# Performance work log

Hardware: AMD Instinct MI355X
Metric: run time of the kernel (lower is better)

The kernel has to match this reference:

```python
import jax, jax.numpy as jnp
import numpy as np

WINDOW_SIZE = 11
C1 = 0.01 ** 2
C2 = 0.03 ** 2


def _box_filter(x, ws):
    # x: [B,1,H,W]; uniform box filter, zero padding (== torch conv2d pad=ws//2)
    k = jnp.full((1, 1, ws, ws), 1.0 / (ws * ws), dtype=x.dtype)
    pad = ws // 2
    return jax.lax.conv_general_dilated(
        x, k, window_strides=(1, 1), padding=[(pad, pad), (pad, pad)],
        dimension_numbers=('NCHW', 'OIHW', 'NCHW'))


def setup_inputs() -> dict:
    key = jax.random.key(0)
    k1, k2 = jax.random.split(key)
    img1 = jax.random.uniform(k1, (64, 1, 512, 512), dtype=jnp.float32)
    img2 = jax.random.uniform(k2, (64, 1, 512, 512), dtype=jnp.float32)
    return {"img1": img1, "img2": img2}


def reference(img1, img2):
    ws = WINDOW_SIZE
    mu1 = _box_filter(img1, ws)
    mu2 = _box_filter(img2, ws)
    mu1_sq = mu1 * mu1
    mu2_sq = mu2 * mu2
    mu1_mu2 = mu1 * mu2
    sigma1_sq = _box_filter(img1 * img1, ws) - mu1_sq
    sigma2_sq = _box_filter(img2 * img2, ws) - mu2_sq
    sigma12 = _box_filter(img1 * img2, ws) - mu1_mu2
    ssim_map = ((2 * mu1_mu2 + C1) * (2 * sigma12 + C2)) / (
        (mu1_sq + mu2_sq + C1) * (sigma1_sq + sigma2_sq + C2))
    return 1.0 - jnp.mean(ssim_map)
```

## Files before the change

kernel.cpp:

```cpp
#include <hip/hip_runtime.h>


#define IMG_H 512
#define IMG_W 512
#define N_IMG 64
#define STRIP 16
#define CHUNK 2
#define NTHREADS 128
#define SSZ 528
#define QSZ 132
#define ROWSZ (SSZ + QSZ)

__global__ __launch_bounds__(NTHREADS) void ssim_kernel(const float* __restrict__ img1,
                                                        const float* __restrict__ img2,
                                                        float* __restrict__ ws) {
    __shared__ __align__(16) float V[CHUNK][4][ROWSZ];
    __shared__ float wsum[2];
    const int t = threadIdx.x;
    const int b = blockIdx.y;
    const int r0 = blockIdx.x * STRIP;
    const float* __restrict__ p1 = img1 + (size_t)b * (IMG_H * IMG_W);
    const float* __restrict__ p2 = img2 + (size_t)b * (IMG_H * IMG_W);

    for (int i = t; i < CHUNK * 4 * ROWSZ; i += NTHREADS) (&V[0][0][0])[i] = 0.0f;

    const int c4 = 4 * t;
    float cs[4][4];
#pragma unroll
    for (int ch = 0; ch < 4; ++ch)
#pragma unroll
        for (int j = 0; j < 4; ++j) cs[ch][j] = 0.0f;

    auto addrow = [&](int r) {
        float4 x = *(const float4*)(p1 + (size_t)r * IMG_W + c4);
        float4 y = *(const float4*)(p2 + (size_t)r * IMG_W + c4);
        float xs[4] = {x.x, x.y, x.z, x.w}, ys[4] = {y.x, y.y, y.z, y.w};
#pragma unroll
        for (int j = 0; j < 4; ++j) {
            float u = xs[j] + ys[j], v = xs[j] - ys[j];
            cs[0][j] += u;                  cs[1][j] += v;
            cs[2][j] = fmaf(u, u, cs[2][j]); cs[3][j] = fmaf(v, v, cs[3][j]);
        }
    };
    auto subrow = [&](int r) {
        float4 x = *(const float4*)(p1 + (size_t)r * IMG_W + c4);
        float4 y = *(const float4*)(p2 + (size_t)r * IMG_W + c4);
        float xs[4] = {x.x, x.y, x.z, x.w}, ys[4] = {y.x, y.y, y.z, y.w};
#pragma unroll
        for (int j = 0; j < 4; ++j) {
            float u = xs[j] + ys[j], v = xs[j] - ys[j];
            cs[0][j] -= u;                  cs[1][j] -= v;
            cs[2][j] = fmaf(-u, u, cs[2][j]); cs[3][j] = fmaf(-v, v, cs[3][j]);
        }
    };

    int offS[4][3], offQ[4][2];
#pragma unroll
    for (int k = 0; k < 4; ++k) {
        const int c = t + 128 * k;
        const int rho = c & 3;
        int e0, e1, e2;
        if (rho == 0)      { e0 = -5; e1 =  4; e2 =  5; }
        else if (rho == 1) { e0 =  3; e1 =  4; e2 =  5; }
        else if (rho == 2) { e0 = -5; e1 = -4; e2 = -3; }
        else               { e0 = -5; e1 = -4; e2 =  5; }
        offS[k][0] = c + 8 + e0; offS[k][1] = c + 8 + e1; offS[k][2] = c + 8 + e2;
        const int mlo = (c >> 2) + ((rho < 2) ? -1 : 0);
        offQ[k][0] = SSZ + 2 + mlo; offQ[k][1] = SSZ + 3 + mlo;
    }

    {
        int rlo = r0 - 5; if (rlo < 0) rlo = 0;
        int rhi = r0 + 5; if (rhi > IMG_H - 1) rhi = IMG_H - 1;
        for (int r = rlo; r <= rhi; ++r) addrow(r);
    }
    __syncthreads();

    constexpr float inv  = 1.0f / 121.0f;
    constexpr float inv2 = 0.5f / 121.0f;
    constexpr float C1c = 0.01f * 0.01f;
    constexpr float C2c = 0.03f * 0.03f;
    float acc = 0.0f;
    const float* __restrict__ Vf = &V[0][0][0];

    for (int rc = r0; rc < r0 + STRIP; rc += CHUNK) {
#pragma unroll
        for (int q = 0; q < CHUNK; ++q) {
            const int r = rc + q;
            if (r > r0) {
                int ri = r + 5, ro = r - 6;
                if (ri < IMG_H) addrow(ri);
                if (ro >= 0)    subrow(ro);
            }
#pragma unroll
            for (int ch = 0; ch < 4; ++ch) {
                *(float4*)&V[q][ch][8 + c4] =
                    make_float4(cs[ch][0], cs[ch][1], cs[ch][2], cs[ch][3]);
                V[q][ch][SSZ + 2 + t] = (cs[ch][0] + cs[ch][1]) + (cs[ch][2] + cs[ch][3]);
            }
        }
        __syncthreads();

#pragma unroll
        for (int q = 0; q < CHUNK; ++q) {
#pragma unroll
            for (int k = 0; k < 4; ++k) {
                float W[4];
#pragma unroll
                for (int ch = 0; ch < 4; ++ch) {
                    const int base = (q * 4 + ch) * ROWSZ;
                    W[ch] = ((Vf[base + offS[k][0]] + Vf[base + offS[k][1]]) +
                             (Vf[base + offS[k][2]] + Vf[base + offQ[k][0]])) +
                            Vf[base + offQ[k][1]];
                }
                float mu_u = W[0] * inv, mu_v = W[1] * inv;
                float uu = mu_u * mu_u, vv = mu_v * mu_v;
                float P = 0.5f * (uu + vv);
                float M = 0.5f * (uu - vv);
                float A = fmaf(W[2] + W[3], inv2, -P);
                float B = fmaf(W[2] - W[3], inv2, -M);
                float num = (M + C1c) * (B + C2c);
                float den = (P + C1c) * (A + C2c);
                acc += __fdividef(num, den);
            }
        }
        __syncthreads();
    }

#pragma unroll
    for (int off = 32; off > 0; off >>= 1) acc += __shfl_down(acc, off);
    if ((t & 63) == 0) wsum[t >> 6] = acc;
    __syncthreads();
    if (t == 0) atomicAdd(ws, wsum[0] + wsum[1]);
}

__global__ void ssim_finalize(const float* __restrict__ ws, float* __restrict__ out) {
    constexpr float inv_n = 1.0f / (float)((size_t)N_IMG * IMG_H * IMG_W);
    out[0] = 1.0f - ws[0] * inv_n;
}

extern "C" void kernel_launch(void* const* d_in, const int* in_sizes, int n_in,
                              void* d_out, int out_size, void* d_ws, size_t ws_size,
                              hipStream_t stream) {
    const float* img1 = (const float*)d_in[0];
    const float* img2 = (const float*)d_in[1];
    float* out = (float*)d_out;
    float* ws = (float*)d_ws;

    hipMemsetAsync(ws, 0, sizeof(float), stream);

    dim3 grid(IMG_H / STRIP, N_IMG);
    ssim_kernel<<<grid, NTHREADS, 0, stream>>>(img1, img2, ws);
    ssim_finalize<<<1, 1, 0, stream>>>(ws, out);
}
```

Measured before the change: 199.5 us.

## Software-pipeline row loads with register prefetch and double-buffered shared rows

Restructures the sliding-window loop so the global loads for the next row go into registers before the horizontal-filter phase of the current row runs. Those loads can then overlap with the shared-memory stencil work. Column sums are written into alternating shared buffers, so each row needs only one barrier, replacing the earlier two-row chunk with a compute/write split. This adds a few registers for the prefetched float4s and a per-row barrier in exchange for hiding global memory latency.

```diff
diff --git a/kernel.cpp b/kernel.cpp
--- a/kernel.cpp
+++ b/kernel.cpp
@@ -5,7 +5,6 @@
 #define IMG_W 512
 #define N_IMG 64
 #define STRIP 16
-#define CHUNK 2
 #define NTHREADS 128
 #define SSZ 528
 #define QSZ 132
@@ -14,7 +13,7 @@
 __global__ __launch_bounds__(NTHREADS) void ssim_kernel(const float* __restrict__ img1,
                                                         const float* __restrict__ img2,
                                                         float* __restrict__ ws) {
-    __shared__ __align__(16) float V[CHUNK][4][ROWSZ];
+    __shared__ __align__(16) float V[2][4][ROWSZ];
     __shared__ float wsum[2];
     const int t = threadIdx.x;
     const int b = blockIdx.y;
@@ -22,7 +21,7 @@
     const float* __restrict__ p1 = img1 + (size_t)b * (IMG_H * IMG_W);
     const float* __restrict__ p2 = img2 + (size_t)b * (IMG_H * IMG_W);
 
-    for (int i = t; i < CHUNK * 4 * ROWSZ; i += NTHREADS) (&V[0][0][0])[i] = 0.0f;
+    for (int i = t; i < 2 * 4 * ROWSZ; i += NTHREADS) (&V[0][0][0])[i] = 0.0f;
 
     const int c4 = 4 * t;
     float cs[4][4];
@@ -42,15 +41,49 @@
             cs[2][j] = fmaf(u, u, cs[2][j]); cs[3][j] = fmaf(v, v, cs[3][j]);
         }
     };
-    auto subrow = [&](int r) {
-        float4 x = *(const float4*)(p1 + (size_t)r * IMG_W + c4);
-        float4 y = *(const float4*)(p2 + (size_t)r * IMG_W + c4);
-        float xs[4] = {x.x, x.y, x.z, x.w}, ys[4] = {y.x, y.y, y.z, y.w};
+
+    float4 pax, pay, psx, psy;
+    auto prefetch = [&](int rn) {
+        if (rn >= r0 + STRIP) return;
+        const int ra = rn + 5, rs = rn - 6;
+        if (ra < IMG_H) {
+            pax = *(const float4*)(p1 + (size_t)ra * IMG_W + c4);
+            pay = *(const float4*)(p2 + (size_t)ra * IMG_W + c4);
+        }
+        if (rs >= 0) {
+            psx = *(const float4*)(p1 + (size_t)rs * IMG_W + c4);
+            psy = *(const float4*)(p2 + (size_t)rs * IMG_W + c4);
+        }
+    };
+    auto consume = [&](int rn) {
+        const int ra = rn + 5, rs = rn - 6;
+        if (ra < IMG_H) {
+            float xs[4] = {pax.x, pax.y, pax.z, pax.w};
+            float ys[4] = {pay.x, pay.y, pay.z, pay.w};
 #pragma unroll
-        for (int j = 0; j < 4; ++j) {
-            float u = xs[j] + ys[j], v = xs[j] - ys[j];
-            cs[0][j] -= u;                  cs[1][j] -= v;
-            cs[2][j] = fmaf(-u, u, cs[2][j]); cs[3][j] = fmaf(-v, v, cs[3][j]);
+            for (int j = 0; j < 4; ++j) {
+                float u = xs[j] + ys[j], v = xs[j] - ys[j];
+                cs[0][j] += u;                  cs[1][j] += v;
+                cs[2][j] = fmaf(u, u, cs[2][j]); cs[3][j] = fmaf(v, v, cs[3][j]);
+            }
+        }
+        if (rs >= 0) {
+            float xs[4] = {psx.x, psx.y, psx.z, psx.w};
+            float ys[4] = {psy.x, psy.y, psy.z, psy.w};
+#pragma unroll
+            for (int j = 0; j < 4; ++j) {
+                float u = xs[j] + ys[j], v = xs[j] - ys[j];
+                cs[0][j] -= u;                  cs[1][j] -= v;
+                cs[2][j] = fmaf(-u, u, cs[2][j]); cs[3][j] = fmaf(-v, v, cs[3][j]);
+            }
+        }
+    };
+    auto writeSQ = [&](int p) {
+#pragma unroll
+        for (int ch = 0; ch < 4; ++ch) {
+            *(float4*)&V[p][ch][8 + c4] =
+                make_float4(cs[ch][0], cs[ch][1], cs[ch][2], cs[ch][3]);
+            V[p][ch][SSZ + 2 + t] = (cs[ch][0] + cs[ch][1]) + (cs[ch][2] + cs[ch][3]);
         }
     };
 
@@ -71,9 +104,12 @@
 
     {
         int rlo = r0 - 5; if (rlo < 0) rlo = 0;
-        int rhi = r0 + 5; if (rhi > IMG_H - 1) rhi = IMG_H - 1;
+        const int rhi = r0 + 5;
         for (int r = rlo; r <= rhi; ++r) addrow(r);
     }
+    __syncthreads();
+    writeSQ(0);
+    prefetch(r0 + 1);
     __syncthreads();
 
     constexpr float inv  = 1.0f / 121.0f;
@@ -81,51 +117,39 @@
     constexpr float C1c = 0.01f * 0.01f;
     constexpr float C2c = 0.03f * 0.03f;
     float acc = 0.0f;
-    const float* __restrict__ Vf = &V[0][0][0];
 
-    for (int rc = r0; rc < r0 + STRIP; rc += CHUNK) {
+    auto hphase = [&](int p) {
+        const float* __restrict__ Vf = &V[p][0][0];
 #pragma unroll
-        for (int q = 0; q < CHUNK; ++q) {
-            const int r = rc + q;
-            if (r > r0) {
-                int ri = r + 5, ro = r - 6;
-                if (ri < IMG_H) addrow(ri);
-                if (ro >= 0)    subrow(ro);
-            }
+        for (int k = 0; k < 4; ++k) {
+            float W[4];
 #pragma unroll
             for (int ch = 0; ch < 4; ++ch) {
-                *(float4*)&V[q][ch][8 + c4] =
-                    make_float4(cs[ch][0], cs[ch][1], cs[ch][2], cs[ch][3]);
-                V[q][ch][SSZ + 2 + t] = (cs[ch][0] + cs[ch][1]) + (cs[ch][2] + cs[ch][3]);
+                const int base = ch * ROWSZ;
+                W[ch] = ((Vf[base + offS[k][0]] + Vf[base + offS[k][1]]) +
+                         (Vf[base + offS[k][2]] + Vf[base + offQ[k][0]])) +
+                        Vf[base + offQ[k][1]];
             }
+            float mu_u = W[0] * inv, mu_v = W[1] * inv;
+            float uu = mu_u * mu_u, vv = mu_v * mu_v;
+            float P = 0.5f * (uu + vv);
+            float M = 0.5f * (uu - vv);
+            float A = fmaf(W[2] + W[3], inv2, -P);
+            float B = fmaf(W[2] - W[3], inv2, -M);
+            float num = (M + C1c) * (B + C2c);
+            float den = (P + C1c) * (A + C2c);
+            acc += __fdividef(num, den);
         }
-        __syncthreads();
+    };
 
-#pragma unroll
-        for (int q = 0; q < CHUNK; ++q) {
-#pragma unroll
-            for (int k = 0; k < 4; ++k) {
-                float W[4];
-#pragma unroll
-                for (int ch = 0; ch < 4; ++ch) {
-                    const int base = (q * 4 + ch) * ROWSZ;
-                    W[ch] = ((Vf[base + offS[k][0]] + Vf[base + offS[k][1]]) +
-                             (Vf[base + offS[k][2]] + Vf[base + offQ[k][0]])) +
-                            Vf[base + offQ[k][1]];
-                }
-                float mu_u = W[0] * inv, mu_v = W[1] * inv;
-                float uu = mu_u * mu_u, vv = mu_v * mu_v;
-                float P = 0.5f * (uu + vv);
-                float M = 0.5f * (uu - vv);
-                float A = fmaf(W[2] + W[3], inv2, -P);
-                float B = fmaf(W[2] - W[3], inv2, -M);
-                float num = (M + C1c) * (B + C2c);
-                float den = (P + C1c) * (A + C2c);
-                acc += __fdividef(num, den);
-            }
-        }
+    for (int i = 0; i < STRIP - 1; ++i) {
+        hphase(i & 1);
+        consume(r0 + i + 1);
+        prefetch(r0 + i + 2);
+        writeSQ((i + 1) & 1);
         __syncthreads();
     }
+    hphase((STRIP - 1) & 1);
 
 #pragma unroll
     for (int off = 32; off > 0; off >>= 1) acc += __shfl_down(acc, off);
```

Result: faster. 191.8 us (-3.8%).

## Replace shared-memory horizontal box sum with register prefix sums and wave shuffles

Applied to the files above, without the earlier changes.

Each thread now holds 8 columns and a single 64-thread wave covers a full row. The horizontal 11-tap sum is built from in-register prefix and suffix sums plus neighbour values fetched with shuffles, replacing the shared-memory staging and the block barriers. The strip height is halved to 8 rows, which gives more blocks and more redundant halo row loads. The next row's load is also prefetched a step ahead. Register pressure rises from 8-column accumulators and the W arrays, which could reduce occupancy.

```diff
diff --git a/kernel.cpp b/kernel.cpp
--- a/kernel.cpp
+++ b/kernel.cpp
@@ -4,134 +4,133 @@
 #define IMG_H 512
 #define IMG_W 512
 #define N_IMG 64
-#define STRIP 16
-#define CHUNK 2
-#define NTHREADS 128
-#define SSZ 528
-#define QSZ 132
-#define ROWSZ (SSZ + QSZ)
+#define STRIP 8
+#define NTHREADS 64
 
-__global__ __launch_bounds__(NTHREADS) void ssim_kernel(const float* __restrict__ img1,
-                                                        const float* __restrict__ img2,
-                                                        float* __restrict__ ws) {
-    __shared__ __align__(16) float V[CHUNK][4][ROWSZ];
-    __shared__ float wsum[2];
+__global__ __launch_bounds__(NTHREADS, 2) void ssim_kernel(const float* __restrict__ img1,
+                                                           const float* __restrict__ img2,
+                                                           float* __restrict__ ws) {
     const int t = threadIdx.x;
     const int b = blockIdx.y;
     const int r0 = blockIdx.x * STRIP;
     const float* __restrict__ p1 = img1 + (size_t)b * (IMG_H * IMG_W);
     const float* __restrict__ p2 = img2 + (size_t)b * (IMG_H * IMG_W);
+    const int c8 = 8 * t;
 
-    for (int i = t; i < CHUNK * 4 * ROWSZ; i += NTHREADS) (&V[0][0][0])[i] = 0.0f;
-
-    const int c4 = 4 * t;
-    float cs[4][4];
+    float cs[4][8];
 #pragma unroll
     for (int ch = 0; ch < 4; ++ch)
 #pragma unroll
-        for (int j = 0; j < 4; ++j) cs[ch][j] = 0.0f;
+        for (int j = 0; j < 8; ++j) cs[ch][j] = 0.0f;
 
-    auto addrow = [&](int r) {
-        float4 x = *(const float4*)(p1 + (size_t)r * IMG_W + c4);
-        float4 y = *(const float4*)(p2 + (size_t)r * IMG_W + c4);
-        float xs[4] = {x.x, x.y, x.z, x.w}, ys[4] = {y.x, y.y, y.z, y.w};
+    auto addR = [&](float4 xa, float4 xb, float4 ya, float4 yb) {
+        float xs[8] = {xa.x, xa.y, xa.z, xa.w, xb.x, xb.y, xb.z, xb.w};
+        float ys[8] = {ya.x, ya.y, ya.z, ya.w, yb.x, yb.y, yb.z, yb.w};
 #pragma unroll
-        for (int j = 0; j < 4; ++j) {
+        for (int j = 0; j < 8; ++j) {
             float u = xs[j] + ys[j], v = xs[j] - ys[j];
-            cs[0][j] += u;                  cs[1][j] += v;
+            cs[0][j] += u;                   cs[1][j] += v;
             cs[2][j] = fmaf(u, u, cs[2][j]); cs[3][j] = fmaf(v, v, cs[3][j]);
         }
     };
-    auto subrow = [&](int r) {
-        float4 x = *(const float4*)(p1 + (size_t)r * IMG_W + c4);
-        float4 y = *(const float4*)(p2 + (size_t)r * IMG_W + c4);
-        float xs[4] = {x.x, x.y, x.z, x.w}, ys[4] = {y.x, y.y, y.z, y.w};
+    auto subR = [&](float4 xa, float4 xb, float4 ya, float4 yb) {
+        float xs[8] = {xa.x, xa.y, xa.z, xa.w, xb.x, xb.y, xb.z, xb.w};
+        float ys[8] = {ya.x, ya.y, ya.z, ya.w, yb.x, yb.y, yb.z, yb.w};
 #pragma unroll
-        for (int j = 0; j < 4; ++j) {
+        for (int j = 0; j < 8; ++j) {
             float u = xs[j] + ys[j], v = xs[j] - ys[j];
-            cs[0][j] -= u;                  cs[1][j] -= v;
+            cs[0][j] -= u;                    cs[1][j] -= v;
             cs[2][j] = fmaf(-u, u, cs[2][j]); cs[3][j] = fmaf(-v, v, cs[3][j]);
         }
     };
 
-    int offS[4][3], offQ[4][2];
-#pragma unroll
-    for (int k = 0; k < 4; ++k) {
-        const int c = t + 128 * k;
-        const int rho = c & 3;
-        int e0, e1, e2;
-        if (rho == 0)      { e0 = -5; e1 =  4; e2 =  5; }
-        else if (rho == 1) { e0 =  3; e1 =  4; e2 =  5; }
-        else if (rho == 2) { e0 = -5; e1 = -4; e2 = -3; }
-        else               { e0 = -5; e1 = -4; e2 =  5; }
-        offS[k][0] = c + 8 + e0; offS[k][1] = c + 8 + e1; offS[k][2] = c + 8 + e2;
-        const int mlo = (c >> 2) + ((rho < 2) ? -1 : 0);
-        offQ[k][0] = SSZ + 2 + mlo; offQ[k][1] = SSZ + 3 + mlo;
+    {
+        int rlo = r0 - 5; if (rlo < 0) rlo = 0;
+        const int rhi = r0 + 5;
+        for (int r = rlo; r <= rhi; ++r) {
+            const float* a1 = p1 + (size_t)r * IMG_W + c8;
+            const float* a2 = p2 + (size_t)r * IMG_W + c8;
+            addR(*(const float4*)a1, *(const float4*)(a1 + 4),
+                 *(const float4*)a2, *(const float4*)(a2 + 4));
+        }
     }
 
-    {
-        int rlo = r0 - 5; if (rlo < 0) rlo = 0;
-        int rhi = r0 + 5; if (rhi > IMG_H - 1) rhi = IMG_H - 1;
-        for (int r = rlo; r <= rhi; ++r) addrow(r);
-    }
-    __syncthreads();
+    float4 fxa, fxb, fya, fyb;
+    auto prefetchAdd = [&](int rn) {
+        int ra = rn + 5; if (ra > IMG_H - 1) ra = IMG_H - 1;
+        const float* a1 = p1 + (size_t)ra * IMG_W + c8;
+        const float* a2 = p2 + (size_t)ra * IMG_W + c8;
+        fxa = *(const float4*)a1; fxb = *(const float4*)(a1 + 4);
+        fya = *(const float4*)a2; fyb = *(const float4*)(a2 + 4);
+    };
 
+    const float mL = (t > 0)  ? 1.0f : 0.0f;
+    const float mR = (t < 63) ? 1.0f : 0.0f;
     constexpr float inv  = 1.0f / 121.0f;
     constexpr float inv2 = 0.5f / 121.0f;
     constexpr float C1c = 0.01f * 0.01f;
     constexpr float C2c = 0.03f * 0.03f;
     float acc = 0.0f;
-    const float* __restrict__ Vf = &V[0][0][0];
 
-    for (int rc = r0; rc < r0 + STRIP; rc += CHUNK) {
+    prefetchAdd(r0 + 1);
+
+    for (int i = 0; i < STRIP; ++i) {
+        float W[4][8];
 #pragma unroll
-        for (int q = 0; q < CHUNK; ++q) {
-            const int r = rc + q;
-            if (r > r0) {
-                int ri = r + 5, ro = r - 6;
-                if (ri < IMG_H) addrow(ri);
-                if (ro >= 0)    subrow(ro);
-            }
-#pragma unroll
-            for (int ch = 0; ch < 4; ++ch) {
-                *(float4*)&V[q][ch][8 + c4] =
-                    make_float4(cs[ch][0], cs[ch][1], cs[ch][2], cs[ch][3]);
-                V[q][ch][SSZ + 2 + t] = (cs[ch][0] + cs[ch][1]) + (cs[ch][2] + cs[ch][3]);
-            }
+        for (int ch = 0; ch < 4; ++ch) {
+            float s0 = cs[ch][0], s1 = cs[ch][1], s2 = cs[ch][2], s3 = cs[ch][3];
+            float s4 = cs[ch][4], s5 = cs[ch][5], s6 = cs[ch][6], s7 = cs[ch][7];
+            float P2 = s0 + s1, P3 = P2 + s2, P4 = P3 + s3, P5 = P4 + s4;
+            float P6 = P5 + s5, P7 = P6 + s6, P8 = P7 + s7;
+            float Q2 = s7 + s6, Q3 = Q2 + s5, Q4 = Q3 + s4, Q5 = Q4 + s3;
+            float Lq1 = __shfl_up(s7, 1), Lq2 = __shfl_up(Q2, 1),
+                  Lq3 = __shfl_up(Q3, 1), Lq4 = __shfl_up(Q4, 1),
+                  Lq5 = __shfl_up(Q5, 1);
+            float Rp1 = __shfl_down(s0, 1), Rp2 = __shfl_down(P2, 1),
+                  Rp3 = __shfl_down(P3, 1), Rp4 = __shfl_down(P4, 1),
+                  Rp5 = __shfl_down(P5, 1);
+            W[ch][0] = fmaf(Lq5, mL, P6);
+            W[ch][1] = fmaf(Lq4, mL, P7);
+            W[ch][2] = fmaf(Lq3, mL, P8);
+            W[ch][3] = fmaf(Rp1, mR, fmaf(Lq2, mL, P8));
+            W[ch][4] = fmaf(Rp2, mR, fmaf(Lq1, mL, P8));
+            W[ch][5] = fmaf(Rp3, mR, P8);
+            W[ch][6] = fmaf(Rp4, mR, P8 - s0);
+            W[ch][7] = fmaf(Rp5, mR, P8 - P2);
         }
-        __syncthreads();
+
+        const int rn = r0 + i + 1;
+        const bool last = (i == STRIP - 1);
+        const bool doSub = !last && (rn - 6 >= 0);
+        float4 sxa, sxb, sya, syb;
+        if (doSub) {
+            const float* a1 = p1 + (size_t)(rn - 6) * IMG_W + c8;
+            const float* a2 = p2 + (size_t)(rn - 6) * IMG_W + c8;
+            sxa = *(const float4*)a1; sxb = *(const float4*)(a1 + 4);
+            sya = *(const float4*)a2; syb = *(const float4*)(a2 + 4);
+        }
 
 #pragma unroll
-        for (int q = 0; q < CHUNK; ++q) {
-#pragma unroll
-            for (int k = 0; k < 4; ++k) {
-                float W[4];
-#pragma unroll
-                for (int ch = 0; ch < 4; ++ch) {
-                    const int base = (q * 4 + ch) * ROWSZ;
-                    W[ch] = ((Vf[base + offS[k][0]] + Vf[base + offS[k][1]]) +
-                             (Vf[base + offS[k][2]] + Vf[base + offQ[k][0]])) +
-                            Vf[base + offQ[k][1]];
-                }
-                float mu_u = W[0] * inv, mu_v = W[1] * inv;
-                float uu = mu_u * mu_u, vv = mu_v * mu_v;
-                float P = 0.5f * (uu + vv);
-                float M = 0.5f * (uu - vv);
-                float A = fmaf(W[2] + W[3], inv2, -P);
-                float B = fmaf(W[2] - W[3], inv2, -M);
-                float num = (M + C1c) * (B + C2c);
-                float den = (P + C1c) * (A + C2c);
-                acc += __fdividef(num, den);
-            }
+        for (int j = 0; j < 8; ++j) {
+            float mu_u = W[0][j] * inv, mu_v = W[1][j] * inv;
+            float uu = mu_u * mu_u, vv = mu_v * mu_v;
+            float Pq = 0.5f * (uu + vv);
+            float Mq = 0.5f * (uu - vv);
+            float A = fmaf(W[2][j] + W[3][j], inv2, -Pq);
+            float B = fmaf(W[2][j] - W[3][j], inv2, -Mq);
+            acc += __fdividef((Mq + C1c) * (B + C2c), (Pq + C1c) * (A + C2c));
         }
-        __syncthreads();
+
+        if (!last) {
+            if (rn + 5 < IMG_H) addR(fxa, fxb, fya, fyb);
+            if (doSub)          subR(sxa, sxb, sya, syb);
+            if (i < STRIP - 2)  prefetchAdd(rn + 1);
+        }
     }
 
 #pragma unroll
     for (int off = 32; off > 0; off >>= 1) acc += __shfl_down(acc, off);
-    if ((t & 63) == 0) wsum[t >> 6] = acc;
-    __syncthreads();
-    if (t == 0) atomicAdd(ws, wsum[0] + wsum[1]);
+    if (t == 0) atomicAdd(ws, acc);
 }
 
 __global__ void ssim_finalize(const float* __restrict__ ws, float* __restrict__ out) {
```

Measured after the change: 215.6 us. 1.08x slower.

## Replace shared-memory horizontal box sum with per-thread overlapping global loads and prefetch

Applied to the files above, without the earlier changes.

Removes the LDS staging of vertical column sums and the block barriers. Each thread now loads a 14-wide horizontal halo of raw pixels per row straight from global memory and applies the horizontal 11-tap window with prefix sums in registers. It keeps a running vertical window by adding and subtracting whole rows, and prefetches the next add row one iteration ahead. This trades LDS traffic and syncs for about 2.5x redundant global or L2 loads, many more ALU ops per row (the horizontal sum is redone for each added and each subtracted row), and higher register pressure under launch_bounds(128,2). The block reduction now uses one atomic per wavefront instead of a shared-memory combine.

```diff
diff --git a/kernel.cpp b/kernel.cpp
--- a/kernel.cpp
+++ b/kernel.cpp
@@ -5,133 +5,133 @@
 #define IMG_W 512
 #define N_IMG 64
 #define STRIP 16
-#define CHUNK 2
 #define NTHREADS 128
-#define SSZ 528
-#define QSZ 132
-#define ROWSZ (SSZ + QSZ)
 
-__global__ __launch_bounds__(NTHREADS) void ssim_kernel(const float* __restrict__ img1,
-                                                        const float* __restrict__ img2,
-                                                        float* __restrict__ ws) {
-    __shared__ __align__(16) float V[CHUNK][4][ROWSZ];
-    __shared__ float wsum[2];
+__global__ __launch_bounds__(NTHREADS, 2) void ssim_kernel(const float* __restrict__ img1,
+                                                           const float* __restrict__ img2,
+                                                           float* __restrict__ ws) {
     const int t = threadIdx.x;
     const int b = blockIdx.y;
     const int r0 = blockIdx.x * STRIP;
     const float* __restrict__ p1 = img1 + (size_t)b * (IMG_H * IMG_W);
     const float* __restrict__ p2 = img2 + (size_t)b * (IMG_H * IMG_W);
+    const int c4 = 4 * t;
 
-    for (int i = t; i < CHUNK * 4 * ROWSZ; i += NTHREADS) (&V[0][0][0])[i] = 0.0f;
+    const int oA = (c4 - 8 > 0) ? c4 - 8 : 0;
+    const int oB = (c4 - 4 > 0) ? c4 - 4 : 0;
+    const int oC = c4;
+    const int oD = (c4 + 4 < 508) ? c4 + 4 : 508;
+    const int oE = (c4 + 8 < 508) ? c4 + 8 : 508;
+    const float fA = (c4 - 5 >= 0) ? 1.0f : 0.0f;
+    const float fB = (c4 - 4 >= 0) ? 1.0f : 0.0f;
+    const float fD = (c4 + 7 <= IMG_W - 1) ? 1.0f : 0.0f;
+    const float fE = (c4 + 8 <= IMG_W - 1) ? 1.0f : 0.0f;
 
-    const int c4 = 4 * t;
-    float cs[4][4];
+    struct Row { float4 A1, B1, C1, D1, E1, A2, B2, C2, D2, E2; };
+    auto issueRow = [&](int r, Row& R) {
+        const float* q1 = p1 + (size_t)r * IMG_W;
+        const float* q2 = p2 + (size_t)r * IMG_W;
+        R.A1 = *(const float4*)(q1 + oA); R.B1 = *(const float4*)(q1 + oB);
+        R.C1 = *(const float4*)(q1 + oC); R.D1 = *(const float4*)(q1 + oD);
+        R.E1 = *(const float4*)(q1 + oE);
+        R.A2 = *(const float4*)(q2 + oA); R.B2 = *(const float4*)(q2 + oB);
+        R.C2 = *(const float4*)(q2 + oC); R.D2 = *(const float4*)(q2 + oD);
+        R.E2 = *(const float4*)(q2 + oE);
+    };
+
+    float Wt[4][4];
 #pragma unroll
     for (int ch = 0; ch < 4; ++ch)
 #pragma unroll
-        for (int j = 0; j < 4; ++j) cs[ch][j] = 0.0f;
+        for (int j = 0; j < 4; ++j) Wt[ch][j] = 0.0f;
 
-    auto addrow = [&](int r) {
-        float4 x = *(const float4*)(p1 + (size_t)r * IMG_W + c4);
-        float4 y = *(const float4*)(p2 + (size_t)r * IMG_W + c4);
-        float xs[4] = {x.x, x.y, x.z, x.w}, ys[4] = {y.x, y.y, y.z, y.w};
+    auto applyRow = [&](const Row& R, const float sgn) {
+        float xs[14], ys[14];
+        xs[0] = R.A1.w * fA;
+        xs[1] = R.B1.x * fB; xs[2] = R.B1.y * fB; xs[3] = R.B1.z * fB; xs[4] = R.B1.w * fB;
+        xs[5] = R.C1.x;      xs[6] = R.C1.y;      xs[7] = R.C1.z;      xs[8] = R.C1.w;
+        xs[9] = R.D1.x * fD; xs[10] = R.D1.y * fD; xs[11] = R.D1.z * fD; xs[12] = R.D1.w * fD;
+        xs[13] = R.E1.x * fE;
+        ys[0] = R.A2.w * fA;
+        ys[1] = R.B2.x * fB; ys[2] = R.B2.y * fB; ys[3] = R.B2.z * fB; ys[4] = R.B2.w * fB;
+        ys[5] = R.C2.x;      ys[6] = R.C2.y;      ys[7] = R.C2.z;      ys[8] = R.C2.w;
+        ys[9] = R.D2.x * fD; ys[10] = R.D2.y * fD; ys[11] = R.D2.z * fD; ys[12] = R.D2.w * fD;
+        ys[13] = R.E2.x * fE;
+        float u[14], v[14];
+#pragma unroll
+        for (int k = 0; k < 14; ++k) { u[k] = xs[k] + ys[k]; v[k] = xs[k] - ys[k]; }
+        float pu[14], pv[14], puu[14], pvv[14];
+        pu[0] = u[0]; pv[0] = v[0];
+        puu[0] = u[0] * u[0]; pvv[0] = v[0] * v[0];
+#pragma unroll
+        for (int k = 1; k < 14; ++k) {
+            pu[k] = pu[k - 1] + u[k];
+            pv[k] = pv[k - 1] + v[k];
+            puu[k] = fmaf(u[k], u[k], puu[k - 1]);
+            pvv[k] = fmaf(v[k], v[k], pvv[k - 1]);
+        }
 #pragma unroll
         for (int j = 0; j < 4; ++j) {
-            float u = xs[j] + ys[j], v = xs[j] - ys[j];
-            cs[0][j] += u;                  cs[1][j] += v;
-            cs[2][j] = fmaf(u, u, cs[2][j]); cs[3][j] = fmaf(v, v, cs[3][j]);
-        }
-    };
-    auto subrow = [&](int r) {
-        float4 x = *(const float4*)(p1 + (size_t)r * IMG_W + c4);
-        float4 y = *(const float4*)(p2 + (size_t)r * IMG_W + c4);
-        float xs[4] = {x.x, x.y, x.z, x.w}, ys[4] = {y.x, y.y, y.z, y.w};
-#pragma unroll
-        for (int j = 0; j < 4; ++j) {
-            float u = xs[j] + ys[j], v = xs[j] - ys[j];
-            cs[0][j] -= u;                  cs[1][j] -= v;
-            cs[2][j] = fmaf(-u, u, cs[2][j]); cs[3][j] = fmaf(-v, v, cs[3][j]);
+            const float w0 = (j == 0) ? pu[10]  : pu[j + 10]  - pu[j - 1];
+            const float w1 = (j == 0) ? pv[10]  : pv[j + 10]  - pv[j - 1];
+            const float w2 = (j == 0) ? puu[10] : puu[j + 10] - puu[j - 1];
+            const float w3 = (j == 0) ? pvv[10] : pvv[j + 10] - pvv[j - 1];
+            Wt[0][j] = fmaf(sgn, w0, Wt[0][j]);
+            Wt[1][j] = fmaf(sgn, w1, Wt[1][j]);
+            Wt[2][j] = fmaf(sgn, w2, Wt[2][j]);
+            Wt[3][j] = fmaf(sgn, w3, Wt[3][j]);
         }
     };
 
-    int offS[4][3], offQ[4][2];
-#pragma unroll
-    for (int k = 0; k < 4; ++k) {
-        const int c = t + 128 * k;
-        const int rho = c & 3;
-        int e0, e1, e2;
-        if (rho == 0)      { e0 = -5; e1 =  4; e2 =  5; }
-        else if (rho == 1) { e0 =  3; e1 =  4; e2 =  5; }
-        else if (rho == 2) { e0 = -5; e1 = -4; e2 = -3; }
-        else               { e0 = -5; e1 = -4; e2 =  5; }
-        offS[k][0] = c + 8 + e0; offS[k][1] = c + 8 + e1; offS[k][2] = c + 8 + e2;
-        const int mlo = (c >> 2) + ((rho < 2) ? -1 : 0);
-        offQ[k][0] = SSZ + 2 + mlo; offQ[k][1] = SSZ + 3 + mlo;
-    }
-
     {
         int rlo = r0 - 5; if (rlo < 0) rlo = 0;
-        int rhi = r0 + 5; if (rhi > IMG_H - 1) rhi = IMG_H - 1;
-        for (int r = rlo; r <= rhi; ++r) addrow(r);
+        const int rhi = r0 + 5;
+        for (int r = rlo; r <= rhi; ++r) {
+            Row R; issueRow(r, R); applyRow(R, 1.0f);
+        }
     }
-    __syncthreads();
 
     constexpr float inv  = 1.0f / 121.0f;
     constexpr float inv2 = 0.5f / 121.0f;
     constexpr float C1c = 0.01f * 0.01f;
     constexpr float C2c = 0.03f * 0.03f;
     float acc = 0.0f;
-    const float* __restrict__ Vf = &V[0][0][0];
 
-    for (int rc = r0; rc < r0 + STRIP; rc += CHUNK) {
-#pragma unroll
-        for (int q = 0; q < CHUNK; ++q) {
-            const int r = rc + q;
-            if (r > r0) {
-                int ri = r + 5, ro = r - 6;
-                if (ri < IMG_H) addrow(ri);
-                if (ro >= 0)    subrow(ro);
-            }
-#pragma unroll
-            for (int ch = 0; ch < 4; ++ch) {
-                *(float4*)&V[q][ch][8 + c4] =
-                    make_float4(cs[ch][0], cs[ch][1], cs[ch][2], cs[ch][3]);
-                V[q][ch][SSZ + 2 + t] = (cs[ch][0] + cs[ch][1]) + (cs[ch][2] + cs[ch][3]);
-            }
-        }
-        __syncthreads();
+    Row nextAdd;
+    { int ra = r0 + 6; if (ra > IMG_H - 1) ra = IMG_H - 1; issueRow(ra, nextAdd); }
+
+    for (int i = 0; i < STRIP; ++i) {
+        const int r = r0 + i;
+        const bool lastIt = (i == STRIP - 1);
+
+        Row subR;
+        const bool doSub = !lastIt && (r - 5 >= 0);
+        if (doSub) issueRow(r - 5, subR);
 
 #pragma unroll
-        for (int q = 0; q < CHUNK; ++q) {
-#pragma unroll
-            for (int k = 0; k < 4; ++k) {
-                float W[4];
-#pragma unroll
-                for (int ch = 0; ch < 4; ++ch) {
-                    const int base = (q * 4 + ch) * ROWSZ;
-                    W[ch] = ((Vf[base + offS[k][0]] + Vf[base + offS[k][1]]) +
-                             (Vf[base + offS[k][2]] + Vf[base + offQ[k][0]])) +
-                            Vf[base + offQ[k][1]];
-                }
-                float mu_u = W[0] * inv, mu_v = W[1] * inv;
-                float uu = mu_u * mu_u, vv = mu_v * mu_v;
-                float P = 0.5f * (uu + vv);
-                float M = 0.5f * (uu - vv);
-                float A = fmaf(W[2] + W[3], inv2, -P);
-                float B = fmaf(W[2] - W[3], inv2, -M);
-                float num = (M + C1c) * (B + C2c);
-                float den = (P + C1c) * (A + C2c);
-                acc += __fdividef(num, den);
+        for (int j = 0; j < 4; ++j) {
+            float mu_u = Wt[0][j] * inv, mu_v = Wt[1][j] * inv;
+            float uu = mu_u * mu_u, vv = mu_v * mu_v;
+            float P = 0.5f * (uu + vv);
+            float M = 0.5f * (uu - vv);
+            float A = fmaf(Wt[2][j] + Wt[3][j], inv2, -P);
+            float B = fmaf(Wt[2][j] - Wt[3][j], inv2, -M);
+            acc += __fdividef((M + C1c) * (B + C2c), (P + C1c) * (A + C2c));
+        }
+
+        if (!lastIt) {
+            if (r + 6 <= IMG_H - 1) applyRow(nextAdd, 1.0f);
+            if (i < STRIP - 2) {
+                int ra = r + 7; if (ra > IMG_H - 1) ra = IMG_H - 1;
+                issueRow(ra, nextAdd);
             }
+            if (doSub) applyRow(subR, -1.0f);
         }
-        __syncthreads();
     }
 
 #pragma unroll
     for (int off = 32; off > 0; off >>= 1) acc += __shfl_down(acc, off);
-    if ((t & 63) == 0) wsum[t >> 6] = acc;
-    __syncthreads();
-    if (t == 0) atomicAdd(ws, wsum[0] + wsum[1]);
+    if ((t & 63) == 0) atomicAdd(ws, acc);
 }
 
 __global__ void ssim_finalize(const float* __restrict__ ws, float* __restrict__ out) {
```

New measurement: 230.8 us. 1.16x slower.
